# Optimization experiments

Measured on AMD Instinct MI355X. Metric: run time of the kernel, lower is better.

Reference implementation:

```python
import jax, jax.numpy as jnp
import numpy as np

N_Q = 5000
MEM = 50
KDIM = 50
VDIM = 200
FC = 50
B = 2048
S = 200


def setup_inputs() -> dict:
    key = jax.random.key(0)
    ks = jax.random.split(key, 14)
    inp = {}
    inp["q_data"] = jax.random.randint(ks[0], (B, S), 0, N_Q, dtype=jnp.int64)
    inp["qa_data"] = jax.random.randint(ks[1], (B, S), 0, 2 * N_Q, dtype=jnp.int64)
    # learned parameters (kaiming-ish random init)
    inp["q_embed_w"] = jax.random.normal(ks[2], (N_Q + 1, KDIM), jnp.float32) * 0.2
    inp["qa_embed_w"] = jax.random.normal(ks[3], (2 * N_Q + 1, VDIM), jnp.float32) * 0.1
    inp["key_memory"] = jax.random.normal(ks[4], (MEM, KDIM), jnp.float32) * 0.2
    inp["init_value_memory"] = jax.random.normal(ks[5], (MEM, VDIM), jnp.float32) * 0.1
    # DKVMN write gates: erase (sigmoid) and add (tanh) transforms of qa embedding
    inp["erase_w"] = jax.random.normal(ks[6], (VDIM, VDIM), jnp.float32) * 0.1
    inp["erase_b"] = jnp.zeros((VDIM,), jnp.float32)
    inp["add_w"] = jax.random.normal(ks[7], (VDIM, VDIM), jnp.float32) * 0.1
    inp["add_b"] = jnp.zeros((VDIM,), jnp.float32)
    # prediction MLP: Linear(VDIM+KDIM -> FC), Tanh, Linear(FC -> 1)
    inp["pred_w1"] = jax.random.normal(ks[8], (VDIM + KDIM, FC), jnp.float32) * 0.1
    inp["pred_b1"] = jnp.zeros((FC,), jnp.float32)
    inp["pred_w2"] = jax.random.normal(ks[9], (FC, 1), jnp.float32) * 0.2
    inp["pred_b2"] = jnp.zeros((1,), jnp.float32)
    return inp


def _dkvmn_forward(q_data, qa_data, q_embed_w, qa_embed_w, key_memory,
                   init_value_memory, erase_w, erase_b, add_w, add_b,
                   pred_w1, pred_b1, pred_w2, pred_b2):
    q_emb = q_embed_w[q_data]    # [B, S, KDIM]
    qa_emb = qa_embed_w[qa_data]  # [B, S, VDIM]
    batch = q_data.shape[0]
    Mv0 = jnp.broadcast_to(init_value_memory, (batch, MEM, VDIM))

    def step(Mv, xs):
        q_t, qa_t = xs  # [B, KDIM], [B, VDIM]
        # attention over memory slots
        w = jax.nn.softmax(q_t @ key_memory.T, axis=-1)          # [B, MEM]
        read = jnp.einsum('bm,bmv->bv', w, Mv)                    # [B, VDIM]
        h = jnp.tanh(jnp.concatenate([read, q_t], -1) @ pred_w1 + pred_b1)
        p = jax.nn.sigmoid((h @ pred_w2 + pred_b2)[:, 0])         # [B]
        # erase/add write
        e = jax.nn.sigmoid(qa_t @ erase_w + erase_b)              # [B, VDIM]
        a = jnp.tanh(qa_t @ add_w + add_b)                        # [B, VDIM]
        Mv_new = Mv * (1.0 - w[:, :, None] * e[:, None, :]) + w[:, :, None] * a[:, None, :]
        return Mv_new, p

    xs = (jnp.swapaxes(q_emb, 0, 1), jnp.swapaxes(qa_emb, 0, 1))  # time-major
    _, preds = jax.lax.scan(step, Mv0, xs)                        # [S, B]
    return preds.T                                                # [B, S]


def reference(q_data, qa_data, q_embed_w, qa_embed_w, key_memory,
              init_value_memory, erase_w, erase_b, add_w, add_b,
              pred_w1, pred_b1, pred_w2, pred_b2):
    preds = _dkvmn_forward(q_data, qa_data, q_embed_w, qa_embed_w, key_memory,
                           init_value_memory, erase_w, erase_b, add_w, add_b,
                           pred_w1, pred_b1, pred_w2, pred_b2)
    zeros = jnp.zeros_like(preds)
    return (preds, zeros, zeros, zeros)
```

## Files before the change

### kernel.cpp

```cpp
#include <hip/hip_runtime.h>


#define NQ1   5001
#define NQA   10001
#define MEMN  50
#define KD    50
#define VD    200
#define FC    50
#define BB    2048
#define SS    200
#define EA_R  16

typedef unsigned int   u32;
typedef unsigned short u16;
typedef short  s8v  __attribute__((ext_vector_type(8)));
typedef float  f4v  __attribute__((ext_vector_type(4)));

__device__ __forceinline__ float fast_sigmoid(float x) { return 1.f / (1.f + __expf(-x)); }
__device__ __forceinline__ float fast_tanh(float x) {
    float e2 = __expf(2.f * x);
    return 1.f - 2.f / (e2 + 1.f);
}
__device__ __forceinline__ float bfu16_to_f(u16 u) {
    union { float f; u32 i; } x; x.i = ((u32)u) << 16; return x.f;
}
__device__ __forceinline__ u16 f_to_bfu16(float f) {
    union { float f; u32 i; } x; x.f = f;
    return (u16)((x.i + 0x7fffu + ((x.i >> 16) & 1u)) >> 16);
}

__global__ void build_wq(const float* __restrict__ qemb,
                         const float* __restrict__ km,
                         const float* __restrict__ w1,
                         const float* __restrict__ b1,
                         float* __restrict__ Wt, float* __restrict__ Q1) {
    const int q = blockIdx.x;
    const int f = threadIdx.x;
    __shared__ float qrow[KD];
    if (f < KD) qrow[f] = qemb[q * KD + f];
    __syncthreads();

    float s = -1e30f;
    if (f < MEMN) {
        s = 0.f;
        #pragma unroll
        for (int k = 0; k < KD; ++k) s = fmaf(qrow[k], km[f * KD + k], s);
    }
    float mx = s;
    #pragma unroll
    for (int off = 32; off >= 1; off >>= 1) mx = fmaxf(mx, __shfl_xor(mx, off, 64));
    float e = (f < MEMN) ? __expf(s - mx) : 0.f;
    float sum = e;
    #pragma unroll
    for (int off = 32; off >= 1; off >>= 1) sum += __shfl_xor(sum, off, 64);
    if (f < MEMN) Wt[q * MEMN + f] = e / sum;

    if (f < FC) {
        float h = b1[f];
        #pragma unroll
        for (int k = 0; k < KD; ++k)
            h = fmaf(qrow[k], w1[(VD + k) * FC + f], h);
        Q1[q * FC + f] = h;
    }
}

__global__ void build_ea(const float* __restrict__ qaemb,
                         const float* __restrict__ ew,
                         const float* __restrict__ ebias,
                         const float* __restrict__ aw,
                         const float* __restrict__ abias,
                         u32* __restrict__ EA) {
    __shared__ float qT[VD][EA_R];
    const int tid = threadIdx.x;
    const int r0 = blockIdx.x * EA_R;
    if (tid < VD) {
        #pragma unroll
        for (int r = 0; r < EA_R; ++r) {
            int row = r0 + r;
            qT[tid][r] = (row < NQA) ? qaemb[(size_t)row * VD + tid] : 0.f;
        }
    }
    __syncthreads();
    if (tid >= VD) return;

    float accE[EA_R], accA[EA_R];
    #pragma unroll
    for (int r = 0; r < EA_R; ++r) { accE[r] = 0.f; accA[r] = 0.f; }
    for (int k = 0; k < VD; ++k) {
        float we = ew[k * VD + tid];
        float wa = aw[k * VD + tid];
        #pragma unroll
        for (int r = 0; r < EA_R; ++r) {
            float qv = qT[k][r];
            accE[r] = fmaf(qv, we, accE[r]);
            accA[r] = fmaf(qv, wa, accA[r]);
        }
    }
    float be = ebias[tid], ba = abias[tid];
    #pragma unroll
    for (int r = 0; r < EA_R; ++r) {
        int row = r0 + r;
        if (row < NQA) {
            u16 e16 = f_to_bfu16(fast_sigmoid(accE[r] + be));
            u16 a16 = f_to_bfu16(fast_tanh(accA[r] + ba));
            EA[(size_t)row * VD + tid] = (u32)e16 | ((u32)a16 << 16);
        }
    }
}

__global__ void pack_w1(const float* __restrict__ w1, u16* __restrict__ W1s) {
    for (int idx = threadIdx.x; idx < 4 * 7 * 64 * 8; idx += blockDim.x) {
        int j    = idx & 7;
        int lane = (idx >> 3) & 63;
        int kt   = (idx >> 9) % 7;
        int nt   = idx / 3584;
        int k = kt * 32 + ((lane >> 4) << 3) + j;
        int n = nt * 16 + (lane & 15);
        float v = (k < VD && n < FC) ? w1[k * FC + n] : 0.f;
        W1s[idx] = f_to_bfu16(v);
    }
}

__global__ __launch_bounds__(256) void dkvmn_state(
        const int* __restrict__ qd, const int* __restrict__ qad,
        const float* __restrict__ Wtab, const u32* __restrict__ EA,
        const float* __restrict__ ivm, u16* __restrict__ READ) {
    const int tid = threadIdx.x;
    const int b   = blockIdx.x;
    const int v   = tid;
    const bool active = v < VD;
    const int vc = active ? v : VD - 1;

    float mv[MEMN];
    #pragma unroll
    for (int m = 0; m < MEMN; ++m) mv[m] = ivm[m * VD + vc];

    const int base = b * SS;
    int q_c = __builtin_amdgcn_readfirstlane(qd[base]);
    int q_n = __builtin_amdgcn_readfirstlane(qd[base + 1]);
    int qa0 = __builtin_amdgcn_readfirstlane(qad[base]);
    int qa1 = __builtin_amdgcn_readfirstlane(qad[base + 1]);
    u32 ea_c = EA[(size_t)qa0 * VD + vc];
    u32 ea_n = EA[(size_t)qa1 * VD + vc];

    for (int t = 0; t < SS; ++t) {
        int q_nn = 0, qa_nn = 0;
        if (t + 2 < SS) {
            q_nn  = __builtin_amdgcn_readfirstlane(qd[base + t + 2]);
            qa_nn = __builtin_amdgcn_readfirstlane(qad[base + t + 2]);
        }
        u32 ea_nn = EA[(size_t)qa_nn * VD + vc];

        const float* wrow = Wtab + q_c * MEMN;
        float ev = bfu16_to_f((u16)(ea_c & 0xffffu));
        float av = bfu16_to_f((u16)(ea_c >> 16));

        float rd0 = 0.f, rd1 = 0.f;
        #pragma unroll
        for (int m = 0; m < MEMN; m += 2) {
            float wm0 = wrow[m], wm1 = wrow[m + 1];
            float m0 = mv[m], m1 = mv[m + 1];
            rd0 = fmaf(wm0, m0, rd0);
            mv[m]     = fmaf(wm0, fmaf(-ev, m0, av), m0);
            rd1 = fmaf(wm1, m1, rd1);
            mv[m + 1] = fmaf(wm1, fmaf(-ev, m1, av), m1);
        }
        if (active)
            READ[(size_t)(base + t) * VD + v] = f_to_bfu16(rd0 + rd1);
        q_c = q_n; q_n = q_nn; ea_c = ea_n; ea_n = ea_nn;
    }
}

__global__ __launch_bounds__(256) void mlp_pred(
        const u16* __restrict__ RD, const int* __restrict__ qd,
        const float* __restrict__ Q1tab, const u16* __restrict__ W1s,
        const float* __restrict__ w2, const float* __restrict__ b2,
        float* __restrict__ out) {
    const int tid  = threadIdx.x;
    const int lane = tid & 63;
    const int wv   = tid >> 6;
    const int strip = blockIdx.x * 4 + wv;
    const int row0  = strip * 16;

    const int mrow = lane & 15;
    const int quad = lane >> 4;

    s8v a[7];
    {
        const u16* arow = RD + (size_t)(row0 + mrow) * VD + quad * 8;
        #pragma unroll
        for (int kt = 0; kt < 7; ++kt)
            a[kt] = *(const s8v*)(arow + kt * 32);
    }

    const float b2f = b2[0];
    float pf[4] = {0.f, 0.f, 0.f, 0.f};

    #pragma unroll
    for (int nt = 0; nt < 4; ++nt) {
        s8v bfr[7];
        #pragma unroll
        for (int kt = 0; kt < 7; ++kt)
            bfr[kt] = *(const s8v*)(W1s + (((nt * 7 + kt) * 64) + lane) * 8);

        f4v acc = {0.f, 0.f, 0.f, 0.f};
        #pragma unroll
        for (int kt = 0; kt < 7; ++kt)
            acc = __builtin_amdgcn_mfma_f32_16x16x32_bf16(a[kt], bfr[kt], acc, 0, 0, 0);

        const int f = nt * 16 + mrow;
        const float w2f = (f < FC) ? w2[f] : 0.f;
        #pragma unroll
        for (int r = 0; r < 4; ++r) {
            int row = row0 + quad * 4 + r;
            float h = acc[r] + Q1tab[qd[row] * FC + f];
            pf[r] = fmaf(fast_tanh(h), w2f, pf[r]);
        }
    }

    #pragma unroll
    for (int r = 0; r < 4; ++r) {
        float s = pf[r];
        s += __shfl_xor(s, 1, 64);
        s += __shfl_xor(s, 2, 64);
        s += __shfl_xor(s, 4, 64);
        s += __shfl_xor(s, 8, 64);
        if (mrow == 0)
            out[row0 + quad * 4 + r] = fast_sigmoid(s + b2f);
    }
}

__global__ void dkvmn_main(const int* __restrict__ qd, const int* __restrict__ qad,
                           const float* __restrict__ Wtab, const float* __restrict__ Q1tab,
                           const u32* __restrict__ EA,
                           const float* __restrict__ ivm,
                           const float* __restrict__ w1,
                           const float* __restrict__ w2,
                           const float* __restrict__ b2,
                           float* __restrict__ out) {
    const int tid  = threadIdx.x;
    const int b    = blockIdx.x;
    const int v    = tid;
    const int lane = tid & 63;
    const int wv   = tid >> 6;

    __shared__ alignas(16) float read_lds[4 * 52];
    __shared__ alignas(16) float part_lds[4 * 52];

    float mv[MEMN];
    if (v < VD) {
        #pragma unroll
        for (int m = 0; m < MEMN; ++m) mv[m] = ivm[m * VD + v];
    }
    float w1r[50];
    if (lane < FC) {
        #pragma unroll
        for (int i = 0; i < 50; ++i) w1r[i] = w1[(wv * 50 + i) * FC + lane];
    } else {
        #pragma unroll
        for (int i = 0; i < 50; ++i) w1r[i] = 0.f;
    }
    const float w2f = (tid < FC) ? w2[tid] : 0.f;
    const float b2f = b2[0];

    const int* qrow_i  = qd  + b * SS;
    const int* qarow_i = qad + b * SS;
    const int jchunk = v / 50;
    const int wslot  = jchunk * 52 + (v - jchunk * 50);

    for (int t = 0; t < SS; ++t) {
        const int q  = __builtin_amdgcn_readfirstlane(qrow_i[t]);
        const int qa = __builtin_amdgcn_readfirstlane(qarow_i[t]);
        const float* wrow = Wtab + q * MEMN;

        u32 ea = 0;
        if (v < VD) ea = EA[(size_t)qa * VD + v];
        float ev = bfu16_to_f((u16)(ea & 0xffffu));
        float av = bfu16_to_f((u16)(ea >> 16));

        if (v < VD) {
            float rd0 = 0.f, rd1 = 0.f;
            #pragma unroll
            for (int m = 0; m < MEMN; m += 2) {
                float wm0 = wrow[m], wm1 = wrow[m + 1];
                rd0 = fmaf(wm0, mv[m], rd0);
                mv[m] = fmaf(wm0, fmaf(-ev, mv[m], av), mv[m]);
                rd1 = fmaf(wm1, mv[m + 1], rd1);
                mv[m + 1] = fmaf(wm1, fmaf(-ev, mv[m + 1], av), mv[m + 1]);
            }
            read_lds[wslot] = rd0 + rd1;
        }
        __syncthreads();

        float part = 0.f;
        {
            const float* rlc = read_lds + wv * 52;
            #pragma unroll
            for (int i = 0; i < 48; i += 4) {
                float4 x = *(const float4*)(rlc + i);
                part = fmaf(x.x, w1r[i],     part);
                part = fmaf(x.y, w1r[i + 1], part);
                part = fmaf(x.z, w1r[i + 2], part);
                part = fmaf(x.w, w1r[i + 3], part);
            }
            part = fmaf(rlc[48], w1r[48], part);
            part = fmaf(rlc[49], w1r[49], part);
        }
        if (lane < FC) part_lds[wv * 52 + lane] = part;
        __syncthreads();

        if (wv == 0) {
            float pf = 0.f;
            if (lane < FC) {
                float h = part_lds[lane] + part_lds[52 + lane] +
                          part_lds[104 + lane] + part_lds[156 + lane] +
                          Q1tab[q * FC + lane];
                pf = fast_tanh(h) * w2f;
            }
            #pragma unroll
            for (int off = 32; off >= 1; off >>= 1) pf += __shfl_xor(pf, off, 64);
            if (lane == 0) out[b * SS + t] = fast_sigmoid(pf + b2f);
        }
    }
}

extern "C" void kernel_launch(void* const* d_in, const int* in_sizes, int n_in,
                              void* d_out, int out_size, void* d_ws, size_t ws_size,
                              hipStream_t stream) {
    const int* qd  = (const int*)d_in[0];
    const int* qad = (const int*)d_in[1];
    const float* qemb  = (const float*)d_in[2];
    const float* qaemb = (const float*)d_in[3];
    const float* km    = (const float*)d_in[4];
    const float* ivm   = (const float*)d_in[5];
    const float* ew    = (const float*)d_in[6];
    const float* eb    = (const float*)d_in[7];
    const float* aw    = (const float*)d_in[8];
    const float* ab    = (const float*)d_in[9];
    const float* w1    = (const float*)d_in[10];
    const float* b1    = (const float*)d_in[11];
    const float* w2    = (const float*)d_in[12];
    const float* b2    = (const float*)d_in[13];
    float* out = (float*)d_out;
    (void)in_sizes; (void)n_in; (void)out_size;

    char* ws = (char*)d_ws;
    float* Wt  = (float*)(ws);
    float* Q1  = (float*)(ws + 1000448);
    u32*   EA  = (u32*)  (ws + 2000896);
    u16*   W1s = (u16*)  (ws + 10001920);
    u16*   RD  = (u16*)  (ws + 10034688);
    const size_t need = 10034688ull + 163840000ull + 512ull;

    hipMemsetAsync(out + (size_t)BB * SS, 0, (size_t)3 * BB * SS * sizeof(float), stream);

    build_wq<<<NQ1, 64, 0, stream>>>(qemb, km, w1, b1, Wt, Q1);
    build_ea<<<(NQA + EA_R - 1) / EA_R, 256, 0, stream>>>(qaemb, ew, eb, aw, ab, EA);

    if (ws_size >= need) {
        pack_w1<<<1, 256, 0, stream>>>(w1, W1s);
        dkvmn_state<<<BB, 256, 0, stream>>>(qd, qad, Wt, EA, ivm, RD);
        mlp_pred<<<(BB * SS) / 64, 256, 0, stream>>>(RD, qd, Q1, W1s, w2, b2, out);
    } else {
        dkvmn_main<<<BB, 256, 0, stream>>>(qd, qad, Wt, Q1, EA, ivm, w1, w2, b2, out);
    }
}
```

Before: 501.6 us.

## Fuse MLP prediction into per-batch state kernel and parallelize W1 packing

The separate mlp_pred kernel is removed, and each dkvmn_state block now runs the MFMA-based prediction MLP over its own 200 timesteps right after the recurrence, reading back its READ rows. This drops one kernel launch and is meant to let the READ data be reread while it is likely still in cache. The pack_w1 kernel is spread across 56 blocks instead of one. In exchange, the tail of each state block gains MFMA work, padded strips (200 is not a multiple of 16) waste some lanes, and the larger fused kernel may need more registers.

```diff
diff --git a/kernel.cpp b/kernel.cpp
--- a/kernel.cpp
+++ b/kernel.cpp
@@ -109,7 +109,8 @@
 }
 
 __global__ void pack_w1(const float* __restrict__ w1, u16* __restrict__ W1s) {
-    for (int idx = threadIdx.x; idx < 4 * 7 * 64 * 8; idx += blockDim.x) {
+    for (int idx = blockIdx.x * blockDim.x + threadIdx.x; idx < 4 * 7 * 64 * 8;
+         idx += gridDim.x * blockDim.x) {
         int j    = idx & 7;
         int lane = (idx >> 3) & 63;
         int kt   = (idx >> 9) % 7;
@@ -124,7 +125,10 @@
 __global__ __launch_bounds__(256) void dkvmn_state(
         const int* __restrict__ qd, const int* __restrict__ qad,
         const float* __restrict__ Wtab, const u32* __restrict__ EA,
-        const float* __restrict__ ivm, u16* __restrict__ READ) {
+        const float* __restrict__ ivm, u16* __restrict__ READ,
+        const float* __restrict__ Q1tab, const u16* __restrict__ W1s,
+        const float* __restrict__ w2, const float* __restrict__ b2,
+        float* __restrict__ out) {
     const int tid = threadIdx.x;
     const int b   = blockIdx.x;
     const int v   = tid;
@@ -169,64 +173,63 @@
             READ[(size_t)(base + t) * VD + v] = f_to_bfu16(rd0 + rd1);
         q_c = q_n; q_n = q_nn; ea_c = ea_n; ea_n = ea_nn;
     }
-}
-
-__global__ __launch_bounds__(256) void mlp_pred(
-        const u16* __restrict__ RD, const int* __restrict__ qd,
-        const float* __restrict__ Q1tab, const u16* __restrict__ W1s,
-        const float* __restrict__ w2, const float* __restrict__ b2,
-        float* __restrict__ out) {
-    const int tid  = threadIdx.x;
+
+    __threadfence_block();
+    __syncthreads();
+
     const int lane = tid & 63;
     const int wv   = tid >> 6;
-    const int strip = blockIdx.x * 4 + wv;
-    const int row0  = strip * 16;
-
     const int mrow = lane & 15;
     const int quad = lane >> 4;
-
-    s8v a[7];
-    {
-        const u16* arow = RD + (size_t)(row0 + mrow) * VD + quad * 8;
-        #pragma unroll
-        for (int kt = 0; kt < 7; ++kt)
-            a[kt] = *(const s8v*)(arow + kt * 32);
-    }
-
     const float b2f = b2[0];
-    float pf[4] = {0.f, 0.f, 0.f, 0.f};
-
-    #pragma unroll
-    for (int nt = 0; nt < 4; ++nt) {
-        s8v bfr[7];
-        #pragma unroll
-        for (int kt = 0; kt < 7; ++kt)
-            bfr[kt] = *(const s8v*)(W1s + (((nt * 7 + kt) * 64) + lane) * 8);
-
-        f4v acc = {0.f, 0.f, 0.f, 0.f};
-        #pragma unroll
-        for (int kt = 0; kt < 7; ++kt)
-            acc = __builtin_amdgcn_mfma_f32_16x16x32_bf16(a[kt], bfr[kt], acc, 0, 0, 0);
-
-        const int f = nt * 16 + mrow;
-        const float w2f = (f < FC) ? w2[f] : 0.f;
+    const u16* RDb = READ + (size_t)base * VD;
+
+    for (int s = wv; s * 16 < SS; s += 4) {
+        const int lrow0 = s * 16;
+        s8v a[7];
+        {
+            int ar = lrow0 + mrow; if (ar >= SS) ar = SS - 1;
+            const u16* arow = RDb + (size_t)ar * VD + quad * 8;
+            #pragma unroll
+            for (int kt = 0; kt < 7; ++kt)
+                a[kt] = *(const s8v*)(arow + kt * 32);
+        }
+
+        float pf[4] = {0.f, 0.f, 0.f, 0.f};
+        #pragma unroll
+        for (int nt = 0; nt < 4; ++nt) {
+            s8v bfr[7];
+            #pragma unroll
+            for (int kt = 0; kt < 7; ++kt)
+                bfr[kt] = *(const s8v*)(W1s + (((nt * 7 + kt) * 64) + lane) * 8);
+
+            f4v acc = {0.f, 0.f, 0.f, 0.f};
+            #pragma unroll
+            for (int kt = 0; kt < 7; ++kt)
+                acc = __builtin_amdgcn_mfma_f32_16x16x32_bf16(a[kt], bfr[kt], acc, 0, 0, 0);
+
+            const int f = nt * 16 + mrow;
+            const float w2f = (f < FC) ? w2[f] : 0.f;
+            #pragma unroll
+            for (int r = 0; r < 4; ++r) {
+                int lrow = lrow0 + quad * 4 + r;
+                float q1v = (lrow < SS) ? Q1tab[qd[base + lrow] * FC + f] : 0.f;
+                float h = acc[r] + q1v;
+                pf[r] = fmaf(fast_tanh(h), w2f, pf[r]);
+            }
+        }
+
         #pragma unroll
         for (int r = 0; r < 4; ++r) {
-            int row = row0 + quad * 4 + r;
-            float h = acc[r] + Q1tab[qd[row] * FC + f];
-            pf[r] = fmaf(fast_tanh(h), w2f, pf[r]);
-        }
-    }
-
-    #pragma unroll
-    for (int r = 0; r < 4; ++r) {
-        float s = pf[r];
-        s += __shfl_xor(s, 1, 64);
-        s += __shfl_xor(s, 2, 64);
-        s += __shfl_xor(s, 4, 64);
-        s += __shfl_xor(s, 8, 64);
-        if (mrow == 0)
-            out[row0 + quad * 4 + r] = fast_sigmoid(s + b2f);
+            float sv = pf[r];
+            sv += __shfl_xor(sv, 1, 64);
+            sv += __shfl_xor(sv, 2, 64);
+            sv += __shfl_xor(sv, 4, 64);
+            sv += __shfl_xor(sv, 8, 64);
+            int lrow = lrow0 + quad * 4 + r;
+            if (mrow == 0 && lrow < SS)
+                out[base + lrow] = fast_sigmoid(sv + b2f);
+        }
     }
 }
 
@@ -358,9 +361,9 @@
     build_ea<<<(NQA + EA_R - 1) / EA_R, 256, 0, stream>>>(qaemb, ew, eb, aw, ab, EA);
 
     if (ws_size >= need) {
-        pack_w1<<<1, 256, 0, stream>>>(w1, W1s);
-        dkvmn_state<<<BB, 256, 0, stream>>>(qd, qad, Wt, EA, ivm, RD);
-        mlp_pred<<<(BB * SS) / 64, 256, 0, stream>>>(RD, qd, Q1, W1s, w2, b2, out);
+        pack_w1<<<56, 256, 0, stream>>>(w1, W1s);
+        dkvmn_state<<<BB, 256, 0, stream>>>(qd, qad, Wt, EA, ivm, RD,
+                                            Q1, W1s, w2, b2, out);
     } else {
         dkvmn_main<<<BB, 256, 0, stream>>>(qd, qad, Wt, Q1, EA, ivm, w1, w2, b2, out);
     }
```

New measurement: 806.9 us. +60.9%, slower.

## Run DKVMN memory recurrence in packed half2 with fp16 attention table

Applied to the files above, without the earlier changes.

Keeps the per-thread value-memory state as 25 packed half2 registers instead of 50 floats. Builds a second attention-weight table in packed fp16 pairs so the recurrence can use packed fma ops and load half as many weight words per step. Also spreads the W1 packing kernel over 56 blocks instead of one. The aim is to halve ALU and register cost in the serial 200-step loop. The price is fp16 rounding that accumulates across steps in the memory state and read sums, which could push results outside tolerance.

```diff
diff --git a/kernel.cpp b/kernel.cpp
--- a/kernel.cpp
+++ b/kernel.cpp
@@ -1,4 +1,5 @@
 #include <hip/hip_runtime.h>
+#include <hip/hip_fp16.h>
 
 
 #define NQ1   5001
@@ -10,6 +11,7 @@
 #define BB    2048
 #define SS    200
 #define EA_R  16
+#define WHS   28
 
 typedef unsigned int   u32;
 typedef unsigned short u16;
@@ -28,12 +30,16 @@
     union { float f; u32 i; } x; x.f = f;
     return (u16)((x.i + 0x7fffu + ((x.i >> 16) & 1u)) >> 16);
 }
+__device__ __forceinline__ __half2 u32_to_h2(u32 u) {
+    union { u32 i; __half2 h; } x; x.i = u; return x.h;
+}
 
 __global__ void build_wq(const float* __restrict__ qemb,
                          const float* __restrict__ km,
                          const float* __restrict__ w1,
                          const float* __restrict__ b1,
-                         float* __restrict__ Wt, float* __restrict__ Q1) {
+                         float* __restrict__ Wt, u32* __restrict__ Wh,
+                         float* __restrict__ Q1) {
     const int q = blockIdx.x;
     const int f = threadIdx.x;
     __shared__ float qrow[KD];
@@ -53,7 +59,18 @@
     float sum = e;
     #pragma unroll
     for (int off = 32; off >= 1; off >>= 1) sum += __shfl_xor(sum, off, 64);
-    if (f < MEMN) Wt[q * MEMN + f] = e / sum;
+    float wv_ = (f < MEMN) ? (e / sum) : 0.f;
+    if (f < MEMN) Wt[q * MEMN + f] = wv_;
+
+    float plo = __shfl(wv_, 2 * (f & 31), 64);
+    float phi = __shfl(wv_, 2 * (f & 31) + 1, 64);
+    if (f < 25) {
+        union { __half h; u16 u; } lo, hi;
+        lo.h = __float2half(plo); hi.h = __float2half(phi);
+        Wh[q * WHS + f] = (u32)lo.u | ((u32)hi.u << 16);
+    } else if (f < WHS) {
+        Wh[q * WHS + f] = 0;
+    }
 
     if (f < FC) {
         float h = b1[f];
@@ -109,7 +126,8 @@
 }
 
 __global__ void pack_w1(const float* __restrict__ w1, u16* __restrict__ W1s) {
-    for (int idx = threadIdx.x; idx < 4 * 7 * 64 * 8; idx += blockDim.x) {
+    for (int idx = blockIdx.x * blockDim.x + threadIdx.x; idx < 4 * 7 * 64 * 8;
+         idx += gridDim.x * blockDim.x) {
         int j    = idx & 7;
         int lane = (idx >> 3) & 63;
         int kt   = (idx >> 9) % 7;
@@ -123,7 +141,7 @@
 
 __global__ __launch_bounds__(256) void dkvmn_state(
         const int* __restrict__ qd, const int* __restrict__ qad,
-        const float* __restrict__ Wtab, const u32* __restrict__ EA,
+        const u32* __restrict__ Wh, const u32* __restrict__ EA,
         const float* __restrict__ ivm, u16* __restrict__ READ) {
     const int tid = threadIdx.x;
     const int b   = blockIdx.x;
@@ -131,9 +149,11 @@
     const bool active = v < VD;
     const int vc = active ? v : VD - 1;
 
-    float mv[MEMN];
-    #pragma unroll
-    for (int m = 0; m < MEMN; ++m) mv[m] = ivm[m * VD + vc];
+    __half2 mv[25];
+    #pragma unroll
+    for (int i = 0; i < 25; ++i)
+        mv[i] = __floats2half2_rn(ivm[(2 * i) * VD + vc],
+                                  ivm[(2 * i + 1) * VD + vc]);
 
     const int base = b * SS;
     int q_c = __builtin_amdgcn_readfirstlane(qd[base]);
@@ -144,29 +164,34 @@
     u32 ea_n = EA[(size_t)qa1 * VD + vc];
 
     for (int t = 0; t < SS; ++t) {
-        int q_nn = 0, qa_nn = 0;
-        if (t + 2 < SS) {
-            q_nn  = __builtin_amdgcn_readfirstlane(qd[base + t + 2]);
-            qa_nn = __builtin_amdgcn_readfirstlane(qad[base + t + 2]);
-        }
+        int tn = t + 2; tn = (tn < SS) ? tn : (SS - 1);
+        int q_nn  = __builtin_amdgcn_readfirstlane(qd[base + tn]);
+        int qa_nn = __builtin_amdgcn_readfirstlane(qad[base + tn]);
         u32 ea_nn = EA[(size_t)qa_nn * VD + vc];
 
-        const float* wrow = Wtab + q_c * MEMN;
+        const u32* wrow = Wh + q_c * WHS;
         float ev = bfu16_to_f((u16)(ea_c & 0xffffu));
         float av = bfu16_to_f((u16)(ea_c >> 16));
-
-        float rd0 = 0.f, rd1 = 0.f;
-        #pragma unroll
-        for (int m = 0; m < MEMN; m += 2) {
-            float wm0 = wrow[m], wm1 = wrow[m + 1];
-            float m0 = mv[m], m1 = mv[m + 1];
-            rd0 = fmaf(wm0, m0, rd0);
-            mv[m]     = fmaf(wm0, fmaf(-ev, m0, av), m0);
-            rd1 = fmaf(wm1, m1, rd1);
-            mv[m + 1] = fmaf(wm1, fmaf(-ev, m1, av), m1);
-        }
-        if (active)
-            READ[(size_t)(base + t) * VD + v] = f_to_bfu16(rd0 + rd1);
+        __half2 av2 = __float2half2_rn(av);
+        __half2 nev2 = __float2half2_rn(-ev);
+
+        __half2 rdA = __float2half2_rn(0.f), rdB = __float2half2_rn(0.f);
+        #pragma unroll
+        for (int i = 0; i < 25; i += 2) {
+            __half2 w0 = u32_to_h2(wrow[i]);
+            rdA = __hfma2(w0, mv[i], rdA);
+            mv[i] = __hfma2(w0, __hfma2(nev2, mv[i], av2), mv[i]);
+            if (i + 1 < 25) {
+                __half2 w1p = u32_to_h2(wrow[i + 1]);
+                rdB = __hfma2(w1p, mv[i + 1], rdB);
+                mv[i + 1] = __hfma2(w1p, __hfma2(nev2, mv[i + 1], av2), mv[i + 1]);
+            }
+        }
+        if (active) {
+            __half2 s2 = __hadd2(rdA, rdB);
+            float rd = __half2float(__low2half(s2)) + __half2float(__high2half(s2));
+            READ[(size_t)(base + t) * VD + v] = f_to_bfu16(rd);
+        }
         q_c = q_n; q_n = q_nn; ea_c = ea_n; ea_n = ea_nn;
     }
 }
@@ -349,17 +374,18 @@
     float* Q1  = (float*)(ws + 1000448);
     u32*   EA  = (u32*)  (ws + 2000896);
     u16*   W1s = (u16*)  (ws + 10001920);
-    u16*   RD  = (u16*)  (ws + 10034688);
-    const size_t need = 10034688ull + 163840000ull + 512ull;
+    u32*   Wh  = (u32*)  (ws + 10034688);
+    u16*   RD  = (u16*)  (ws + 10595328);
+    const size_t need = 10595328ull + 163840000ull + 512ull;
 
     hipMemsetAsync(out + (size_t)BB * SS, 0, (size_t)3 * BB * SS * sizeof(float), stream);
 
-    build_wq<<<NQ1, 64, 0, stream>>>(qemb, km, w1, b1, Wt, Q1);
+    build_wq<<<NQ1, 64, 0, stream>>>(qemb, km, w1, b1, Wt, Wh, Q1);
     build_ea<<<(NQA + EA_R - 1) / EA_R, 256, 0, stream>>>(qaemb, ew, eb, aw, ab, EA);
 
     if (ws_size >= need) {
-        pack_w1<<<1, 256, 0, stream>>>(w1, W1s);
-        dkvmn_state<<<BB, 256, 0, stream>>>(qd, qad, Wt, EA, ivm, RD);
+        pack_w1<<<56, 256, 0, stream>>>(w1, W1s);
+        dkvmn_state<<<BB, 256, 0, stream>>>(qd, qad, Wh, EA, ivm, RD);
         mlp_pred<<<(BB * SS) / 64, 256, 0, stream>>>(RD, qd, Q1, W1s, w2, b2, out);
     } else {
         dkvmn_main<<<BB, 256, 0, stream>>>(qd, qad, Wt, Q1, EA, ivm, w1, w2, b2, out);
```

Result: faster. 482.3 us (-3.8%).
